# Kernel tuning notes

Hardware: AMD Instinct MI355X
Metric: run time of the kernel (lower is better)

The kernel has to match this reference:

```python
import jax, jax.numpy as jnp
import numpy as np

VAR0, VAR1 = 0.1, 0.2
THRESHOLD = 0.35
NEGPOS_RATIO = 7
LOW_GT_THRESH = 0.2  # match() filters GT whose best prior IoU < 0.2


def setup_inputs() -> dict:
    key = jax.random.key(0)
    ks = jax.random.split(key, 8)
    B, P, G = 16, 43008, 128
    loc_data = jax.random.normal(ks[0], (B, P, 4), jnp.float32)
    conf_data = jax.random.normal(ks[1], (B, P, 2), jnp.float32)
    landm_data = jax.random.normal(ks[2], (B, P, 10), jnp.float32)
    # priors in cxcywh form, positive sizes
    pc = jax.random.uniform(ks[3], (P, 2), jnp.float32)
    pwh = jax.random.uniform(ks[4], (P, 2), jnp.float32, minval=0.02, maxval=0.32)
    priors = jnp.concatenate([pc, pwh], axis=1)
    # targets: valid xyxy boxes + 10 landmark coords + label (face=1)
    ctr = jax.random.uniform(ks[5], (B, G, 2), jnp.float32, minval=0.2, maxval=0.8)
    wh = jax.random.uniform(ks[6], (B, G, 2), jnp.float32, minval=0.05, maxval=0.3)
    boxes = jnp.concatenate([ctr - wh / 2, ctr + wh / 2], axis=-1)
    landms = jax.random.uniform(ks[7], (B, G, 10), jnp.float32)
    labels = jnp.ones((B, G, 1), jnp.float32)
    targets = jnp.concatenate([boxes, landms, labels], axis=-1)
    return {"loc_data": loc_data, "conf_data": conf_data, "landm_data": landm_data,
            "priors": priors, "targets": targets}


def point_form(priors):
    return jnp.concatenate([priors[:, :2] - priors[:, 2:] / 2,
                            priors[:, :2] + priors[:, 2:] / 2], axis=1)


def jaccard(a, b):  # a: [G,4] xyxy, b: [P,4] xyxy -> [G,P]
    lt = jnp.maximum(a[:, None, :2], b[None, :, :2])
    rb = jnp.minimum(a[:, None, 2:], b[None, :, 2:])
    wh = jnp.clip(rb - lt, 0.0)
    inter = wh[..., 0] * wh[..., 1]
    area_a = (a[:, 2] - a[:, 0]) * (a[:, 3] - a[:, 1])
    area_b = (b[:, 2] - b[:, 0]) * (b[:, 3] - b[:, 1])
    return inter / (area_a[:, None] + area_b[None, :] - inter)


def encode(matched, priors):  # matched xyxy [P,4], priors cxcywh [P,4]
    g_cxcy = (matched[:, :2] + matched[:, 2:]) / 2 - priors[:, :2]
    g_cxcy = g_cxcy / (VAR0 * priors[:, 2:])
    g_wh = jnp.log((matched[:, 2:] - matched[:, :2]) / priors[:, 2:]) / VAR1
    return jnp.concatenate([g_cxcy, g_wh], axis=1)


def encode_landm(matched, priors):  # matched [P,10], priors [P,4]
    m = matched.reshape(-1, 5, 2)
    g = (m - priors[:, None, :2]) / (VAR0 * priors[:, None, 2:])
    return g.reshape(-1, 10)


def match_one(truths, labels, landms, priors):
    G = truths.shape[0]
    overlaps = jaccard(truths, point_form(priors))  # [G, P]
    best_prior_overlap = overlaps.max(axis=1)       # [G]
    best_prior_idx = overlaps.argmax(axis=1)        # [G]
    valid = best_prior_overlap >= LOW_GT_THRESH
    any_valid = jnp.any(valid)
    best_truth_overlap = overlaps.max(axis=0)       # [P]
    best_truth_idx = overlaps.argmax(axis=0)        # [P]
    # index_fill_(0, best_prior_idx_filter, 2): ensure each valid GT keeps its best prior
    fill_val = jnp.where(valid, 2.0, best_truth_overlap[best_prior_idx])
    best_truth_overlap = best_truth_overlap.at[best_prior_idx].set(fill_val)
    # best_truth_idx[best_prior_idx[j]] = j for all j
    best_truth_idx = best_truth_idx.at[best_prior_idx].set(jnp.arange(G))
    matches = truths[best_truth_idx]                       # [P,4]
    conf = labels[best_truth_idx].astype(jnp.int32)        # [P]
    conf = jnp.where(best_truth_overlap < THRESHOLD, 0, conf)
    conf = jnp.where(any_valid, conf, 0)  # no valid GT -> all background
    loc = encode(matches, priors)
    landm = encode_landm(landms[best_truth_idx], priors)
    return loc, conf, landm


def smooth_l1(x):
    ax = jnp.abs(x)
    return jnp.where(ax < 1.0, 0.5 * ax * ax, ax - 0.5)


def reference(loc_data, conf_data, landm_data, priors, targets):
    truths = targets[..., :4]
    landms = targets[..., 4:14]
    labels = targets[..., 14]
    loc_t, conf_t, landm_t = jax.vmap(
        lambda t, l, lm: match_one(t, l, lm, priors))(truths, labels, landms)

    # landmark loss over positives
    pos1 = conf_t > 0
    N1 = jnp.maximum(pos1.sum().astype(jnp.float32), 1.0)
    loss_landm = jnp.sum(smooth_l1(landm_data - landm_t) * pos1[..., None])

    # localization loss over positives
    pos = conf_t != 0
    num_pos = pos.sum(axis=1, keepdims=True)  # [B,1]
    loss_l = jnp.sum(smooth_l1(loc_data - loc_t) * pos[..., None])

    # hard negative mining on per-prior CE loss
    lse = jax.scipy.special.logsumexp(conf_data, axis=-1)  # [B,P]
    gathered = jnp.take_along_axis(conf_data, conf_t[..., None], axis=-1)[..., 0]
    ce_all = lse - gathered                                # [B,P] per-prior CE
    mine = jnp.where(pos, 0.0, ce_all)
    loss_idx = jnp.argsort(-mine, axis=1)
    idx_rank = jnp.argsort(loss_idx, axis=1)
    num_neg = jnp.clip(NEGPOS_RATIO * num_pos, None, pos.shape[1] - 1)
    neg = idx_rank < num_neg
    sel = pos | neg
    loss_c = jnp.sum(jnp.where(sel, ce_all, 0.0))

    N = jnp.maximum(num_pos.sum().astype(jnp.float32), 1.0)
    return loss_l / N, loss_c / N, loss_landm / N1
```

## Files before the change

### kernel.cpp

```cpp
#include <hip/hip_runtime.h>
#include <stdint.h>


#define GC 8
#define PPI 4
#define NCELL 1024

__device__ __forceinline__ float sl1(float x) {
  float a = fabsf(x);
  return a < 1.f ? 0.5f * a * a : a - 0.5f;
}

__device__ __forceinline__ double dwave(double v) {
#pragma unroll
  for (int o = 32; o; o >>= 1) v += __shfl_down(v, o);
  return v;
}

__device__ __forceinline__ int cellOf(float4 pr) {
  int cx = (int)(pr.x * 16.f); cx = cx < 0 ? 0 : (cx > 15 ? 15 : cx);
  int cy = (int)(pr.y * 16.f); cy = cy < 0 ? 0 : (cy > 15 ? 15 : cy);
  return ((cy * 16 + cx) << 2) | ((pr.z > 0.17f) ? 2 : 0) |
         ((pr.w > 0.17f) ? 1 : 0);
}

__device__ __forceinline__ unsigned bsufscan(unsigned x, unsigned* S,
                                             unsigned* wt, int tid) {
  int lane = tid & 63, wid = tid >> 6;
  unsigned v = x;
#pragma unroll
  for (int o = 1; o < 64; o <<= 1) {
    unsigned u = __shfl_down(v, o);
    if (lane + o < 64) v += u;
  }
  if (lane == 0) wt[wid] = v;
  __syncthreads();
  if (wid == 0) {
    unsigned tv = (lane < 16) ? wt[lane] : 0;
#pragma unroll
    for (int o = 1; o < 16; o <<= 1) {
      unsigned u = __shfl_down(tv, o);
      if (lane + o < 64) tv += u;
    }
    if (lane < 16) wt[lane] = tv;
  }
  __syncthreads();
  unsigned Sv = v + ((wid < 15) ? wt[wid + 1] : 0u);
  S[tid] = Sv;
  __syncthreads();
  return Sv;
}

__global__ __launch_bounds__(256) void k_hist(const float* __restrict__ priors,
                                              unsigned* __restrict__ cellh,
                                              int P) {
  int p = blockIdx.x * 256 + threadIdx.x;
  if (p < P) {
    float4 pr = ((const float4*)priors)[p];
    atomicAdd(&cellh[cellOf(pr)], 1u);
  }
}

__global__ __launch_bounds__(1024) void k_scan(const unsigned* __restrict__ cellh,
                                               unsigned* __restrict__ cellcur) {
  int tid = threadIdx.x;
  __shared__ unsigned s[NCELL];
  unsigned v = cellh[tid];
  s[tid] = v;
  __syncthreads();
  for (int off = 1; off < NCELL; off <<= 1) {
    unsigned a = (tid >= off) ? s[tid - off] : 0u;
    __syncthreads();
    s[tid] += a;
    __syncthreads();
  }
  cellcur[tid] = s[tid] - v;
}

__global__ __launch_bounds__(256) void k_scatter(
    const float* __restrict__ priors, unsigned* __restrict__ cellcur,
    float4* __restrict__ spr, unsigned* __restrict__ sid,
    unsigned* __restrict__ inv, int P) {
  int p = blockIdx.x * 256 + threadIdx.x;
  if (p < P) {
    float4 pr = ((const float4*)priors)[p];
    unsigned pos = atomicAdd(&cellcur[cellOf(pr)], 1u);
    spr[pos] = pr;
    sid[pos] = (unsigned)p;
    inv[p] = pos;
  }
}

__global__ __launch_bounds__(64) void k_wbox(const float4* __restrict__ spr,
                                             float4* __restrict__ wboxG, int P) {
  int p = blockIdx.x * 64 + threadIdx.x;
  float x1 = 1e30f, y1 = 1e30f, x2 = -1e30f, y2 = -1e30f;
  if (p < P) {
    float4 pr = spr[p];
    x1 = pr.x - pr.z * 0.5f; y1 = pr.y - pr.w * 0.5f;
    x2 = pr.x + pr.z * 0.5f; y2 = pr.y + pr.w * 0.5f;
  }
#pragma unroll
  for (int o = 32; o; o >>= 1) {
    x1 = fminf(x1, __shfl_down(x1, o));
    y1 = fminf(y1, __shfl_down(y1, o));
    x2 = fmaxf(x2, __shfl_down(x2, o));
    y2 = fmaxf(y2, __shfl_down(y2, o));
  }
  if (threadIdx.x == 0)
    wboxG[blockIdx.x] = make_float4(x1, y1, x2, y2);
}

__global__ __launch_bounds__(256) void k_gmask(
    const float4* __restrict__ wboxG, const float* __restrict__ targets,
    uint4* __restrict__ gmask, int G, int NRW, int NW) {
  int w = blockIdx.x * 4 + (threadIdx.x >> 6);
  int lane = threadIdx.x & 63;
  if (w >= NW) return;
  int b = w / NRW, run = w % NRW;
  float4 wb = wboxG[run];
  const float* t0 = targets + ((size_t)b * G + lane) * 15;
  const float* t1 = targets + ((size_t)b * G + lane + 64) * 15;
  bool o0, o1;
  {
    float gx1 = t0[0], gy1 = t0[1], gx2 = t0[2], gy2 = t0[3];
    o0 = (gx1 < wb.z) && (wb.x < gx2) && (gy1 < wb.w) && (wb.y < gy2);
  }
  {
    float gx1 = t1[0], gy1 = t1[1], gx2 = t1[2], gy2 = t1[3];
    o1 = (gx1 < wb.z) && (wb.x < gx2) && (gy1 < wb.w) && (wb.y < gy2);
  }
  unsigned long long b0 = __ballot(o0);
  unsigned long long b1 = __ballot(o1);
  if (lane == 0)
    gmask[(size_t)b * NRW + run] =
        make_uint4((unsigned)b0, (unsigned)(b0 >> 32), (unsigned)b1,
                   (unsigned)(b1 >> 32));
}

__global__ __launch_bounds__(256) void k_pconf(
    const float* __restrict__ conf, const unsigned* __restrict__ inv,
    float2* __restrict__ conf_s, int P) {
  int p = blockIdx.x * 256 + threadIdx.x;
  int b = blockIdx.y;
  if (p < P)
    conf_s[(size_t)b * P + inv[p]] = ((const float2*)conf)[(size_t)b * P + p];
}

__global__ __launch_bounds__(256) void k_mm(
    const float4* __restrict__ spr, const unsigned* __restrict__ sid,
    const uint4* __restrict__ gmask, const float2* __restrict__ conf_s,
    const float* __restrict__ targets, const float* __restrict__ loc,
    const float* __restrict__ lm, uint2* __restrict__ ovti,
    unsigned long long* __restrict__ bp, float* __restrict__ mine,
    unsigned* __restrict__ ghist, double* __restrict__ pll,
    double* __restrict__ pllm, double* __restrict__ plc,
    double* __restrict__ msum, int* __restrict__ pnp, int P, int G, int NIOU,
    int PTI, int NGC, int PC, int NRW) {
  int tid = threadIdx.x;
  __shared__ char smem[16384];
  __shared__ float4 sgt[128];
  __shared__ float sga[128];

  if ((int)blockIdx.x < NIOU) {
    float* st = (float*)smem;
    double* rs = (double*)(smem + 7680);
    int* ri = (int*)(smem + 7808);
    unsigned* hist = (unsigned*)(smem + 8192);
    unsigned* smaskw = (unsigned*)(smem + 12288);
    int b = blockIdx.x / PTI, tile = blockIdx.x % PTI;
    int base = tile * (256 * PPI);
    for (int i = tid; i < G * 15; i += 256)
      st[i] = targets[(size_t)b * G * 15 + i];
    for (int g = tid; g < G; g += 256) {
      const float* t = targets + ((size_t)b * G + g) * 15;
      float x1 = t[0], y1 = t[1], x2 = t[2], y2 = t[3];
      sgt[g] = make_float4(x1, y1, x2, y2);
      sga[g] = (x2 - x1) * (y2 - y1);
    }
    for (int i = tid; i < 1024; i += 256) hist[i] = 0;
    if (tid < 64)
      smaskw[tid] =
          ((const unsigned*)(gmask + (size_t)b * NRW + tile * 16))[tid];
    __syncthreads();

    float px1[PPI], py1[PPI], px2[PPI], py2[PPI], pa[PPI];
    float bi[PPI], sb[PPI];
    int bidx[PPI];
#pragma unroll
    for (int k = 0; k < PPI; ++k) {
      int p = base + tid + k * 256;
      int pl = p < P ? p : P - 1;
      float4 pr = spr[pl];
      px1[k] = pr.x - pr.z * 0.5f; py1[k] = pr.y - pr.w * 0.5f;
      px2[k] = pr.x + pr.z * 0.5f; py2[k] = pr.y + pr.w * 0.5f;
      pa[k] = pr.z * pr.w;
      bi[k] = 0.f; sb[k] = 1.f; bidx[k] = 0;
    }

#define IOU_UPD(GG)                                                        \
  {                                                                        \
    float iw = fminf(T.z, px2[k]) - fmaxf(T.x, px1[k]);                    \
    float ih = fminf(T.w, py2[k]) - fmaxf(T.y, py1[k]);                    \
    float inter = fmaxf(iw, 0.f) * ih;                                     \
    float S = A + pa[k];                                                   \
    if (inter * sb[k] > bi[k] * S) { bi[k] = inter; sb[k] = S; bidx[k] = (GG); } \
  }
#pragma unroll
    for (int k = 0; k < PPI; ++k) {
      int runl = k * 4 + (tid >> 6);
      unsigned mw0 = smaskw[runl * 4 + 0], mw1 = smaskw[runl * 4 + 1];
      unsigned mw2 = smaskw[runl * 4 + 2], mw3 = smaskw[runl * 4 + 3];
      unsigned long long m0 =
          ((unsigned long long)(unsigned)__builtin_amdgcn_readfirstlane(
               (int)mw1)
           << 32) |
          (unsigned)__builtin_amdgcn_readfirstlane((int)mw0);
      unsigned long long m1 =
          ((unsigned long long)(unsigned)__builtin_amdgcn_readfirstlane(
               (int)mw3)
           << 32) |
          (unsigned)__builtin_amdgcn_readfirstlane((int)mw2);
      while (m0) {
        int g = __builtin_ctzll(m0);
        m0 &= m0 - 1;
        float4 T = sgt[g];
        float A = sga[g];
        IOU_UPD(g)
      }
      while (m1) {
        int g = 64 + __builtin_ctzll(m1);
        m1 &= m1 - 1;
        float4 T = sgt[g];
        float A = sga[g];
        IOU_UPD(g)
      }
    }
#undef IOU_UPD

    double ll = 0, llm = 0, lc = 0, ms = 0;
    int np = 0;
#pragma unroll
    for (int k = 0; k < PPI; ++k) {
      int p = base + tid + k * 256;
      if (p < P) {
        size_t idxs = (size_t)b * P + p;
        float ov = bi[k] / (sb[k] - bi[k]);
        int ti = bidx[k];
        ovti[idxs] = make_uint2(__float_as_uint(ov), (unsigned)ti);
        bool pos = ov >= 0.35f;
        float2 c = conf_s[idxs];
        float mx = fmaxf(c.x, c.y);
        float dd = fabsf(c.x - c.y);
        float lse = mx + logf(1.f + expf(-dd));
        float ce = lse - (pos ? c.y : c.x);
        float mv = pos ? 0.f : ce;
        mine[idxs] = mv;
        atomicAdd(&hist[__float_as_uint(mv) >> 21], 1u);
        ms += (double)mv;
        if (pos) {
          np++;
          lc += (double)ce;
          float4 pr = spr[p];
          unsigned op = sid[p];
          size_t idxo = (size_t)b * P + op;
          const float* t = st + ti * 15;
          float rz = 1.f / pr.z, rw = 1.f / pr.w;
          float rdx = 10.f * rz, rdy = 10.f * rw;
          float gx = ((t[0] + t[2]) * 0.5f - pr.x) * rdx;
          float gy = ((t[1] + t[3]) * 0.5f - pr.y) * rdy;
          float gw = logf((t[2] - t[0]) * rz) * 5.0f;
          float gh = logf((t[3] - t[1]) * rw) * 5.0f;
          float4 ld = ((const float4*)loc)[idxo];
          ll += (double)(sl1(ld.x - gx) + sl1(ld.y - gy) + sl1(ld.z - gw) +
                         sl1(ld.w - gh));
          const float2* lmd = (const float2*)lm + idxo * 5;
          float s = 0.f;
#pragma unroll
          for (int j = 0; j < 5; ++j) {
            float2 lv = lmd[j];
            float ex = (t[4 + 2 * j] - pr.x) * rdx;
            float ey = (t[5 + 2 * j] - pr.y) * rdy;
            s += sl1(lv.x - ex) + sl1(lv.y - ey);
          }
          llm += (double)s;
        }
      }
    }

    ll = dwave(ll); llm = dwave(llm); lc = dwave(lc); ms = dwave(ms);
#pragma unroll
    for (int o = 32; o; o >>= 1) np += __shfl_down(np, o);
    int lane = tid & 63, wid = tid >> 6;
    if (lane == 0) {
      rs[wid] = ll; rs[4 + wid] = llm; rs[8 + wid] = lc; rs[12 + wid] = ms;
      ri[wid] = np;
    }
    __syncthreads();
    if (tid == 0) {
      pll[blockIdx.x] = rs[0] + rs[1] + rs[2] + rs[3];
      pllm[blockIdx.x] = rs[4] + rs[5] + rs[6] + rs[7];
      plc[blockIdx.x] = rs[8] + rs[9] + rs[10] + rs[11];
      msum[blockIdx.x] = rs[12] + rs[13] + rs[14] + rs[15];
      pnp[blockIdx.x] = ri[0] + ri[1] + ri[2] + ri[3];
    }
    for (int i = tid; i < 1024; i += 256) {
      unsigned c = hist[i];
      if (c) atomicAdd(&ghist[b * 1024 + i], c);
    }
  } else {
    unsigned long long* sred = (unsigned long long*)smem;
    unsigned char* bm = (unsigned char*)sga;
    int bc = blockIdx.x - NIOU;
    int pc = bc % PC;
    int gcb = (bc / PC) % NGC;
    int b = bc / (PC * NGC);
    int g0 = gcb * GC;

    int chunk = (P + PC - 1) / PC;
    int ps = pc * chunk;
    int pe = ps + chunk; if (pe > P) pe = P;
    int count = pe - ps;
    int nrun = (count + 63) >> 6;

    if (tid < GC) {
      int g = g0 + tid;
      float4 v = make_float4(0.f, 0.f, 0.f, 0.f);
      if (g < G) {
        const float* t = targets + ((size_t)b * G + g) * 15;
        v = make_float4(t[0], t[1], t[2], t[3]);
      }
      sgt[tid] = v;
    }
    if (tid < nrun) {
      uint4 m = gmask[(size_t)b * NRW + (ps >> 6) + tid];
      unsigned word = (g0 & 64) ? ((g0 & 32) ? m.w : m.z)
                                : ((g0 & 32) ? m.y : m.x);
      bm[tid] = (unsigned char)((word >> (g0 & 31)) & 0xffu);
    }
    __syncthreads();

    float gx1[GC], gy1[GC], gx2[GC], gy2[GC], ga[GC];
#pragma unroll
    for (int j = 0; j < GC; ++j) {
      float4 T = sgt[j];
      gx1[j] = T.x; gy1[j] = T.y; gx2[j] = T.z; gy2[j] = T.w;
      ga[j] = (T.z - T.x) * (T.w - T.y);
    }

    float bi[GC], sb[GC];
    unsigned bpp[GC];
#pragma unroll
    for (int j = 0; j < GC; ++j) { bi[j] = 0.f; sb[j] = 1.f; bpp[j] = 0xFFFFFFFFu; }

#define BP_BODY(X1, Y1, X2, Y2, AR, PP)                                     \
  {                                                                         \
    float iw = fminf(gx2[j], X2) - fmaxf(gx1[j], X1);                       \
    float ih = fminf(gy2[j], Y2) - fmaxf(gy1[j], Y1);                       \
    float inter = fmaxf(iw, 0.f) * ih;                                      \
    float S = ga[j] + AR;                                                   \
    if (inter * sb[j] > bi[j] * S) { bi[j] = inter; sb[j] = S; bpp[j] = (PP); } \
  }
    for (int i = tid; i < count; i += 1024) {
      int ib = __builtin_amdgcn_readfirstlane(i);
      int rl = ib >> 6;
      int i1 = i + 256, i2 = i + 512, i3 = i + 768;
      int p0 = ps + i;
      int p1 = (i1 < count) ? ps + i1 : p0;
      int p2 = (i2 < count) ? ps + i2 : p0;
      int p3 = (i3 < count) ? ps + i3 : p0;
      unsigned by0 = bm[rl];
      unsigned by1 = bm[(ib + 256 < count) ? rl + 4 : rl];
      unsigned by2 = bm[(ib + 512 < count) ? rl + 8 : rl];
      unsigned by3 = bm[(ib + 768 < count) ? rl + 12 : rl];
      by0 = (unsigned)__builtin_amdgcn_readfirstlane((int)by0);
      by1 = (unsigned)__builtin_amdgcn_readfirstlane((int)by1);
      by2 = (unsigned)__builtin_amdgcn_readfirstlane((int)by2);
      by3 = (unsigned)__builtin_amdgcn_readfirstlane((int)by3);
      float4 q0 = spr[p0];
      float4 q1 = spr[p1];
      float4 q2 = spr[p2];
      float4 q3 = spr[p3];
      unsigned s0 = sid[p0], s1 = sid[p1], s2 = sid[p2], s3 = sid[p3];
      float ax1 = q0.x - q0.z * 0.5f, ay1 = q0.y - q0.w * 0.5f;
      float ax2 = q0.x + q0.z * 0.5f, ay2 = q0.y + q0.w * 0.5f;
      float aa = q0.z * q0.w;
      float bx1 = q1.x - q1.z * 0.5f, by1f = q1.y - q1.w * 0.5f;
      float bx2 = q1.x + q1.z * 0.5f, by2f = q1.y + q1.w * 0.5f;
      float ba = q1.z * q1.w;
      float cx1 = q2.x - q2.z * 0.5f, cy1 = q2.y - q2.w * 0.5f;
      float cx2 = q2.x + q2.z * 0.5f, cy2 = q2.y + q2.w * 0.5f;
      float ca = q2.z * q2.w;
      float dx1 = q3.x - q3.z * 0.5f, dy1 = q3.y - q3.w * 0.5f;
      float dx2 = q3.x + q3.z * 0.5f, dy2 = q3.y + q3.w * 0.5f;
      float da = q3.z * q3.w;
#pragma unroll
      for (int j = 0; j < GC; ++j) {
        if (by0 & (1u << j)) BP_BODY(ax1, ay1, ax2, ay2, aa, s0)
        if (by1 & (1u << j)) BP_BODY(bx1, by1f, bx2, by2f, ba, s1)
        if (by2 & (1u << j)) BP_BODY(cx1, cy1, cx2, cy2, ca, s2)
        if (by3 & (1u << j)) BP_BODY(dx1, dy1, dx2, dy2, da, s3)
      }
    }
#undef BP_BODY

#pragma unroll
    for (int j = 0; j < GC; ++j) {
      float iou = bi[j] / (sb[j] - bi[j]);
      unsigned long long pk =
          ((unsigned long long)__float_as_uint(iou) << 32) | (unsigned)(~bpp[j]);
      sred[j * 256 + tid] = pk;
    }
    __syncthreads();
    {
      int j = tid >> 5, s = tid & 31;
      unsigned long long m = sred[j * 256 + s];
#pragma unroll
      for (int t = 1; t < 8; ++t) {
        unsigned long long v = sred[j * 256 + s + t * 32];
        if (v > m) m = v;
      }
      __syncthreads();
      sred[j * 256 + s] = m;
    }
    __syncthreads();
    if (tid < GC) {
      unsigned long long m = sred[tid * 256];
      for (int s = 1; s < 32; ++s) {
        unsigned long long v = sred[tid * 256 + s];
        if (v > m) m = v;
      }
      int g = g0 + tid;
      if (g < G) atomicMax(&bp[(size_t)b * G + g], m);
    }
  }
}

__global__ __launch_bounds__(1024) void k_tail2(
    const unsigned long long* __restrict__ bp, const unsigned* __restrict__ inv,
    uint2* __restrict__ ovti, const float* __restrict__ conf,
    const float* __restrict__ loc, const float* __restrict__ lm,
    const float* __restrict__ priors, const float* __restrict__ targets,
    float* __restrict__ mine, unsigned* __restrict__ ghist,
    const int* __restrict__ pnp, const double* __restrict__ msum,
    const double* __restrict__ pll, const double* __restrict__ pllm,
    const double* __restrict__ plc, double* __restrict__ gacc,
    int* __restrict__ gnp, unsigned* __restrict__ done,
    float* __restrict__ out, int P, int G, int PTI, int B) {
  int b = blockIdx.x, tid = threadIdx.x;
  int lane = tid & 63, wid = tid >> 6;
  __shared__ unsigned spp[128];
  __shared__ double rs[16 * 5];
  __shared__ int ris[16];
  __shared__ unsigned S[1024];
  __shared__ unsigned hs[2048];
  __shared__ unsigned wt[16];
  __shared__ double sdel[4];
  __shared__ int sdnp, sav, smode;
  __shared__ long long sk;
  __shared__ double sA, sC, sD;
  __shared__ int snpos;
  __shared__ int st_, sk1_;
  __shared__ unsigned lcnt;
  __shared__ int spf21, sk2;
  __shared__ unsigned stb;
  __shared__ double stie;

  double dll = 0, dllm = 0, dlc = 0, dms = 0;
  int dnp = 0;
  unsigned pp = 0;
  bool valid = false;
  if (tid < G) {
    unsigned long long m = bp[(size_t)b * G + tid];
    pp = (m == 0ull) ? 0u : ~(unsigned)m;
    float val = __uint_as_float((unsigned)(m >> 32));
    spp[tid] = pp;
    valid = val >= 0.2f;
  }
  int av = __syncthreads_or((tid < G && valid) ? 1 : 0);
  bool win = false;
  if (tid < G) {
    win = true;
    for (int g2 = tid + 1; g2 < G; ++g2)
      if (spp[g2] == pp) { win = false; break; }
  }
  if (win) {
    size_t idx = (size_t)b * P + pp;
    unsigned sp = inv[pp];
    size_t idxs = (size_t)b * P + sp;
    uint2 ot = ovti[idxs];
    float ov_o = __uint_as_float(ot.x);
    int ti_o = (int)ot.y;
    float ov_n = valid ? 2.0f : ov_o;
    int ti_n = tid;
    bool pos_o = ov_o >= 0.35f, pos_n = ov_n >= 0.35f;

    float2 c = ((const float2*)conf)[idx];
    float mx = fmaxf(c.x, c.y);
    float dd = fabsf(c.x - c.y);
    float lse = mx + logf(1.f + expf(-dd));
    float ce_o = lse - (pos_o ? c.y : c.x);
    float ce_n = lse - (pos_n ? c.y : c.x);
    float mv_o = mine[idxs];
    float mv_n = pos_n ? 0.f : ce_n;
    if (mv_n != mv_o) {
      mine[idxs] = mv_n;
      atomicSub(&ghist[b * 1024 + (__float_as_uint(mv_o) >> 21)], 1u);
      atomicAdd(&ghist[b * 1024 + (__float_as_uint(mv_n) >> 21)], 1u);
    }
    dms = (double)mv_n - (double)mv_o;
    dnp = (pos_n ? 1 : 0) - (pos_o ? 1 : 0);
    dlc = (pos_n ? (double)ce_n : 0.0) - (pos_o ? (double)ce_o : 0.0);

    if (pos_o || pos_n) {
      float4 pr = ((const float4*)priors)[pp];
      float rz = 1.f / pr.z, rw = 1.f / pr.w;
      float rdx = 10.f * rz, rdy = 10.f * rw;
      float4 ld = ((const float4*)loc)[idx];
      const float2* lmd = (const float2*)lm + idx * 5;
      float2 lv[5];
#pragma unroll
      for (int j = 0; j < 5; ++j) lv[j] = lmd[j];
      for (int pass = 0; pass < 2; ++pass) {
        bool act = pass ? pos_n : pos_o;
        int ti = pass ? ti_n : ti_o;
        if (!act) continue;
        const float* t = targets + ((size_t)b * G + ti) * 15;
        float gx = ((t[0] + t[2]) * 0.5f - pr.x) * rdx;
        float gy = ((t[1] + t[3]) * 0.5f - pr.y) * rdy;
        float gw = logf((t[2] - t[0]) * rz) * 5.0f;
        float gh = logf((t[3] - t[1]) * rw) * 5.0f;
        double l = (double)(sl1(ld.x - gx) + sl1(ld.y - gy) +
                            sl1(ld.z - gw) + sl1(ld.w - gh));
        float s = 0.f;
#pragma unroll
        for (int j = 0; j < 5; ++j) {
          float ex = (t[4 + 2 * j] - pr.x) * rdx;
          float ey = (t[5 + 2 * j] - pr.y) * rdy;
          s += sl1(lv[j].x - ex) + sl1(lv[j].y - ey);
        }
        if (pass) { dll += l; dllm += (double)s; }
        else { dll -= l; dllm -= (double)s; }
      }
    }
  }
  dll = dwave(dll); dllm = dwave(dllm); dlc = dwave(dlc); dms = dwave(dms);
#pragma unroll
  for (int o = 32; o; o >>= 1) dnp += __shfl_down(dnp, o);
  if (lane == 0) {
    rs[wid] = dll; rs[16 + wid] = dllm; rs[32 + wid] = dlc; rs[48 + wid] = dms;
    ris[wid] = dnp;
  }
  __syncthreads();
  if (tid == 0) {
    double a = 0, c2 = 0, d2 = 0, m2 = 0;
    int n2 = 0;
    for (int i = 0; i < 16; ++i) {
      a += rs[i]; c2 += rs[16 + i]; d2 += rs[32 + i]; m2 += rs[48 + i];
      n2 += ris[i];
    }
    sdel[0] = a; sdel[1] = c2; sdel[2] = d2; sdel[3] = m2;
    sdnp = n2; sav = av;
  }
  __syncthreads();

  double a = 0, cc = 0, d = 0, ms = 0;
  int n = 0;
  for (int i = tid; i < PTI; i += 1024) {
    int ix = b * PTI + i;
    a += pll[ix]; cc += pllm[ix]; d += plc[ix]; ms += msum[ix]; n += pnp[ix];
  }
  a = dwave(a); cc = dwave(cc); d = dwave(d); ms = dwave(ms);
#pragma unroll
  for (int o = 32; o; o >>= 1) n += __shfl_down(n, o);
  if (lane == 0) {
    rs[wid] = a; rs[16 + wid] = cc; rs[32 + wid] = d; rs[48 + wid] = ms;
    ris[wid] = n;
  }
  __syncthreads();
  double Fv = 0.0;
  if (tid == 0) {
    double A = 0, C = 0, D = 0, MS = 0;
    int npos = 0;
    for (int i = 0; i < 16; ++i) {
      A += rs[i]; C += rs[16 + i]; D += rs[32 + i]; MS += rs[48 + i];
      npos += ris[i];
    }
    A += sdel[0]; C += sdel[1]; D += sdel[2]; MS += sdel[3];
    npos += sdnp;
    if (!sav) { A = 0; C = 0; D = 0; npos = 0; }
    sA = A; sC = C; sD = D; snpos = npos;
    long long k = 7LL * (long long)npos;
    long long cap = P - 1;
    int md = 1;
    if (k <= 0) { Fv = 0.0; md = 0; }
    else if (k >= cap) { Fv = MS; md = 0; }
    smode = md; sk = k;
  }
  __syncthreads();

  if (smode) {
    long long k = sk;
    {
      unsigned x = ghist[b * 1024 + tid];
      unsigned Sv = bsufscan(x, S, wt, tid);
      int cnt_ = __syncthreads_count((long long)Sv >= k);
      int seg = cnt_ - 1;
      if (tid == seg) {
        long long cum = (seg + 1 < 1024) ? (long long)S[seg + 1] : 0;
        st_ = seg;
        sk1_ = (int)(k - cum);
      }
      if (tid == 0) lcnt = 0;
    }
    __syncthreads();
    int t = st_;
    long long k1 = (long long)sk1_;

    const float* mrow = mine + (size_t)b * P;
    float* crow = (float*)(ovti + (size_t)b * P);
    double acc = 0;
    for (int base0 = 0; base0 < P; base0 += 1024) {
      int p = base0 + tid;
      bool keep = false;
      unsigned bb = 0;
      if (p < P) {
        bb = __float_as_uint(mrow[p]);
        int bin = (int)(bb >> 21);
        if (bin > t) acc += (double)__uint_as_float(bb);
        else keep = (bin == t);
      }
      unsigned long long mk = __ballot(keep);
      int nset = __popcll(mk);
      if (nset) {
        unsigned wbase = 0;
        if (lane == 0) wbase = atomicAdd(&lcnt, (unsigned)nset);
        wbase = __shfl(wbase, 0);
        if (keep) {
          int offi = __popcll(mk & ((1ull << lane) - 1ull));
          crow[wbase + offi] = __uint_as_float(bb);
        }
      }
    }
    acc = dwave(acc);
    if (lane == 0) rs[wid] = acc;
    __syncthreads();
    int nn = (int)lcnt;

    hs[tid] = 0; hs[tid + 1024] = 0;
    __syncthreads();
    for (int i = tid; i < nn; i += 1024) {
      unsigned bb = __float_as_uint(crow[i]);
      atomicAdd(&hs[(bb >> 10) & 2047], 1u);
    }
    __syncthreads();
    {
      unsigned h0 = hs[tid * 2], h1v = hs[tid * 2 + 1];
      unsigned Sv = bsufscan(h0 + h1v, S, wt, tid);
      int cnt_ = __syncthreads_count((long long)Sv >= k1);
      int seg = cnt_ - 1;
      if (tid == seg) {
        long long cum = (seg + 1 < 1024) ? (long long)S[seg + 1] : 0;
        int bin = seg * 2;
        if (cum + h1v >= k1) bin = seg * 2 + 1;
        else cum += h1v;
        spf21 = (t << 11) | bin;
        sk2 = (int)(k1 - cum);
      }
    }
    __syncthreads();
    int pf21 = spf21;

    hs[tid] = 0;
    __syncthreads();
    for (int i = tid; i < nn; i += 1024) {
      unsigned bb = __float_as_uint(crow[i]);
      if ((int)(bb >> 10) == pf21) atomicAdd(&hs[bb & 1023], 1u);
    }
    __syncthreads();
    {
      unsigned Sv = bsufscan(hs[tid], S, wt, tid);
      long long kk = (long long)sk2;
      int cnt_ = __syncthreads_count((long long)Sv >= kk);
      int seg = cnt_ - 1;
      if (tid == seg) {
        long long cum = (seg + 1 < 1024) ? (long long)S[seg + 1] : 0;
        unsigned tb = ((unsigned)pf21 << 10) | (unsigned)seg;
        stb = tb;
        stie = (double)(kk - cum) * (double)__uint_as_float(tb);
      }
    }
    __syncthreads();

    unsigned tb = stb;
    double v = 0.0;
    for (int i = tid; i < nn; i += 1024) {
      unsigned bb = __float_as_uint(crow[i]);
      if (bb > tb) v += (double)__uint_as_float(bb);
    }
    v = dwave(v);
    if (lane == 0) rs[16 + wid] = v;
    __syncthreads();
    if (tid == 0) {
      double hi = 0, vt = 0;
      for (int i = 0; i < 16; ++i) { hi += rs[i]; vt += rs[16 + i]; }
      Fv = hi + vt + stie;
    }
  }

  if (tid == 0) {
    atomicAdd(&gacc[0], sA);
    atomicAdd(&gacc[1], sC);
    atomicAdd(&gacc[2], sD);
    atomicAdd(&gacc[3], Fv);
    atomicAdd(gnp, snpos);
    __threadfence();
    unsigned old = atomicAdd(done, 1u);
    if (old == (unsigned)B - 1) {
      __threadfence();
      double A = atomicAdd(&gacc[0], 0.0);
      double C = atomicAdd(&gacc[1], 0.0);
      double D = atomicAdd(&gacc[2], 0.0);
      double F = atomicAdd(&gacc[3], 0.0);
      int N = atomicAdd(gnp, 0);
      double Nd = N < 1 ? 1.0 : (double)N;
      out[0] = (float)(A / Nd);
      out[1] = (float)((D + F) / Nd);
      out[2] = (float)(C / Nd);
    }
  }
}

extern "C" void kernel_launch(void* const* d_in, const int* in_sizes, int n_in,
                              void* d_out, int out_size, void* d_ws,
                              size_t ws_size, hipStream_t stream) {
  const float* loc = (const float*)d_in[0];
  const float* conf = (const float*)d_in[1];
  const float* lm = (const float*)d_in[2];
  const float* priors = (const float*)d_in[3];
  const float* targets = (const float*)d_in[4];

  int P = in_sizes[3] / 4;
  int B = in_sizes[0] / (4 * P);
  int G = in_sizes[4] / (15 * B);
  int PTI = (P + 256 * PPI - 1) / (256 * PPI);
  int NIOU = B * PTI;
  int NGC = (G + GC - 1) / GC;
  int PC = 8;
  int NBP = B * NGC * PC;
  int NPB = (P + 255) / 256;
  int NRW = (P + 63) / 64;
  int NW = B * NRW;

  char* w = (char*)d_ws;
  size_t off = 0;
  unsigned long long* bp = (unsigned long long*)(w + off);
  off += (size_t)B * G * 8;
  unsigned* ghist = (unsigned*)(w + off);
  off += (size_t)B * 1024 * 4;
  unsigned* cellh = (unsigned*)(w + off);
  off += (size_t)NCELL * 4;
  double* gacc = (double*)(w + off);
  off += 4 * 8;
  int* gnp = (int*)(w + off);
  off += 4;
  unsigned* done = (unsigned*)(w + off);
  off += 4;
  size_t clear_bytes = off;
  off = (off + 255) & ~(size_t)255;
  float4* spr = (float4*)(w + off);
  off += (size_t)NRW * 64 * 16;
  unsigned* sid = (unsigned*)(w + off);
  off += (size_t)P * 4;
  unsigned* inv = (unsigned*)(w + off);
  off += (size_t)P * 4;
  float4* wboxG = (float4*)(w + off);
  off += (size_t)NRW * 16;
  uint4* gmask = (uint4*)(w + off);
  off += (size_t)NW * 16;
  unsigned* cellcur = (unsigned*)(w + off);
  off += (size_t)NCELL * 4;
  off = (off + 255) & ~(size_t)255;
  float2* conf_s = (float2*)(w + off);
  off += (size_t)B * P * 8;
  uint2* ovti = (uint2*)(w + off);
  off += (size_t)B * P * 8;
  float* mine = (float*)(w + off);
  off += (size_t)B * P * 4;
  double* pll = (double*)(w + off);
  off += (size_t)NIOU * 8;
  double* pllm = (double*)(w + off);
  off += (size_t)NIOU * 8;
  double* plc = (double*)(w + off);
  off += (size_t)NIOU * 8;
  double* msum = (double*)(w + off);
  off += (size_t)NIOU * 8;
  int* pnp = (int*)(w + off);
  off += (size_t)NIOU * 4;

  hipMemsetAsync(d_ws, 0, clear_bytes, stream);

  k_hist<<<NPB, 256, 0, stream>>>(priors, cellh, P);
  k_scan<<<1, 1024, 0, stream>>>(cellh, cellcur);
  k_scatter<<<NPB, 256, 0, stream>>>(priors, cellcur, spr, sid, inv, P);
  k_wbox<<<NRW, 64, 0, stream>>>(spr, wboxG, P);
  k_gmask<<<(NW + 3) / 4, 256, 0, stream>>>(wboxG, targets, gmask, G, NRW, NW);
  {
    dim3 gp((unsigned)((P + 255) / 256), (unsigned)B);
    k_pconf<<<gp, 256, 0, stream>>>(conf, inv, conf_s, P);
  }
  k_mm<<<NIOU + NBP, 256, 0, stream>>>(spr, sid, gmask, conf_s, targets, loc,
                                       lm, ovti, bp, mine, ghist, pll, pllm,
                                       plc, msum, pnp, P, G, NIOU, PTI, NGC,
                                       PC, NRW);
  k_tail2<<<B, 1024, 0, stream>>>(bp, inv, ovti, conf, loc, lm, priors,
                                  targets, mine, ghist, pnp, msum, pll, pllm,
                                  plc, gacc, gnp, done, (float*)d_out, P, G,
                                  PTI, B);
}
```

Before: 197.6 us.

## Fuse window-box and gmask kernels, drop conf permutation, halve priors per thread

```diff
diff --git a/kernel.cpp b/kernel.cpp
--- a/kernel.cpp
+++ b/kernel.cpp
@@ -3,7 +3,7 @@
 
 
 #define GC 8
-#define PPI 4
+#define PPI 2
 #define NCELL 1024
 
 __device__ __forceinline__ float sl1(float x) {
@@ -91,9 +91,14 @@
   }
 }
 
-__global__ __launch_bounds__(64) void k_wbox(const float4* __restrict__ spr,
-                                             float4* __restrict__ wboxG, int P) {
-  int p = blockIdx.x * 64 + threadIdx.x;
+__global__ __launch_bounds__(64) void k_wgm(
+    const float4* __restrict__ spr, const float* __restrict__ targets,
+    uint4* __restrict__ gmask, unsigned* __restrict__ zbase, int zwords,
+    int G, int NRW, int B, int P) {
+  int run = blockIdx.x, lane = threadIdx.x;
+  for (int i = run * 64 + lane; i < zwords; i += NRW * 64) zbase[i] = 0u;
+
+  int p = run * 64 + lane;
   float x1 = 1e30f, y1 = 1e30f, x2 = -1e30f, y2 = -1e30f;
   if (p < P) {
     float4 pr = spr[p];
@@ -107,49 +112,26 @@
     x2 = fmaxf(x2, __shfl_down(x2, o));
     y2 = fmaxf(y2, __shfl_down(y2, o));
   }
-  if (threadIdx.x == 0)
-    wboxG[blockIdx.x] = make_float4(x1, y1, x2, y2);
-}
-
-__global__ __launch_bounds__(256) void k_gmask(
-    const float4* __restrict__ wboxG, const float* __restrict__ targets,
-    uint4* __restrict__ gmask, int G, int NRW, int NW) {
-  int w = blockIdx.x * 4 + (threadIdx.x >> 6);
-  int lane = threadIdx.x & 63;
-  if (w >= NW) return;
-  int b = w / NRW, run = w % NRW;
-  float4 wb = wboxG[run];
-  const float* t0 = targets + ((size_t)b * G + lane) * 15;
-  const float* t1 = targets + ((size_t)b * G + lane + 64) * 15;
-  bool o0, o1;
-  {
-    float gx1 = t0[0], gy1 = t0[1], gx2 = t0[2], gy2 = t0[3];
-    o0 = (gx1 < wb.z) && (wb.x < gx2) && (gy1 < wb.w) && (wb.y < gy2);
-  }
-  {
-    float gx1 = t1[0], gy1 = t1[1], gx2 = t1[2], gy2 = t1[3];
-    o1 = (gx1 < wb.z) && (wb.x < gx2) && (gy1 < wb.w) && (wb.y < gy2);
-  }
-  unsigned long long b0 = __ballot(o0);
-  unsigned long long b1 = __ballot(o1);
-  if (lane == 0)
-    gmask[(size_t)b * NRW + run] =
-        make_uint4((unsigned)b0, (unsigned)(b0 >> 32), (unsigned)b1,
-                   (unsigned)(b1 >> 32));
-}
-
-__global__ __launch_bounds__(256) void k_pconf(
-    const float* __restrict__ conf, const unsigned* __restrict__ inv,
-    float2* __restrict__ conf_s, int P) {
-  int p = blockIdx.x * 256 + threadIdx.x;
-  int b = blockIdx.y;
-  if (p < P)
-    conf_s[(size_t)b * P + inv[p]] = ((const float2*)conf)[(size_t)b * P + p];
+  x1 = __shfl(x1, 0); y1 = __shfl(y1, 0);
+  x2 = __shfl(x2, 0); y2 = __shfl(y2, 0);
+
+  for (int b = 0; b < B; ++b) {
+    const float* t0 = targets + ((size_t)b * G + lane) * 15;
+    const float* t1 = targets + ((size_t)b * G + lane + 64) * 15;
+    bool o0 = (t0[0] < x2) && (x1 < t0[2]) && (t0[1] < y2) && (y1 < t0[3]);
+    bool o1 = (t1[0] < x2) && (x1 < t1[2]) && (t1[1] < y2) && (y1 < t1[3]);
+    unsigned long long b0 = __ballot(o0);
+    unsigned long long b1 = __ballot(o1);
+    if (lane == 0)
+      gmask[(size_t)b * NRW + run] =
+          make_uint4((unsigned)b0, (unsigned)(b0 >> 32), (unsigned)b1,
+                     (unsigned)(b1 >> 32));
+  }
 }
 
 __global__ __launch_bounds__(256) void k_mm(
     const float4* __restrict__ spr, const unsigned* __restrict__ sid,
-    const uint4* __restrict__ gmask, const float2* __restrict__ conf_s,
+    const uint4* __restrict__ gmask, const float* __restrict__ conf,
     const float* __restrict__ targets, const float* __restrict__ loc,
     const float* __restrict__ lm, uint2* __restrict__ ovti,
     unsigned long long* __restrict__ bp, float* __restrict__ mine,
@@ -179,9 +161,9 @@
       sga[g] = (x2 - x1) * (y2 - y1);
     }
     for (int i = tid; i < 1024; i += 256) hist[i] = 0;
-    if (tid < 64)
+    if (tid < 8 * 4)
       smaskw[tid] =
-          ((const unsigned*)(gmask + (size_t)b * NRW + tile * 16))[tid];
+          ((const unsigned*)(gmask + (size_t)b * NRW + tile * (4 * PPI)))[tid];
     __syncthreads();
 
     float px1[PPI], py1[PPI], px2[PPI], py2[PPI], pa[PPI];
@@ -249,7 +231,9 @@
         int ti = bidx[k];
         ovti[idxs] = make_uint2(__float_as_uint(ov), (unsigned)ti);
         bool pos = ov >= 0.35f;
-        float2 c = conf_s[idxs];
+        unsigned op = sid[p];
+        size_t idxo = (size_t)b * P + op;
+        float2 c = ((const float2*)conf)[idxo];
         float mx = fmaxf(c.x, c.y);
         float dd = fabsf(c.x - c.y);
         float lse = mx + logf(1.f + expf(-dd));
@@ -262,8 +246,6 @@
           np++;
           lc += (double)ce;
           float4 pr = spr[p];
-          unsigned op = sid[p];
-          size_t idxo = (size_t)b * P + op;
           const float* t = st + ti * 15;
           float rz = 1.f / pr.z, rw = 1.f / pr.w;
           float rdx = 10.f * rz, rdy = 10.f * rw;
@@ -620,25 +602,28 @@
     const float* mrow = mine + (size_t)b * P;
     float* crow = (float*)(ovti + (size_t)b * P);
     double acc = 0;
-    for (int base0 = 0; base0 < P; base0 += 1024) {
-      int p = base0 + tid;
-      bool keep = false;
-      unsigned bb = 0;
-      if (p < P) {
-        bb = __float_as_uint(mrow[p]);
-        int bin = (int)(bb >> 21);
-        if (bin > t) acc += (double)__uint_as_float(bb);
-        else keep = (bin == t);
-      }
-      unsigned long long mk = __ballot(keep);
-      int nset = __popcll(mk);
-      if (nset) {
-        unsigned wbase = 0;
-        if (lane == 0) wbase = atomicAdd(&lcnt, (unsigned)nset);
-        wbase = __shfl(wbase, 0);
-        if (keep) {
-          int offi = __popcll(mk & ((1ull << lane) - 1ull));
-          crow[wbase + offi] = __uint_as_float(bb);
+    for (int base0 = 0; base0 < P; base0 += 4096) {
+#pragma unroll
+      for (int j = 0; j < 4; ++j) {
+        int p = base0 + tid + j * 1024;
+        bool keep = false;
+        unsigned bb = 0;
+        if (p < P) {
+          bb = __float_as_uint(mrow[p]);
+          int bin = (int)(bb >> 21);
+          if (bin > t) acc += (double)__uint_as_float(bb);
+          else keep = (bin == t);
+        }
+        unsigned long long mk = __ballot(keep);
+        int nset = __popcll(mk);
+        if (nset) {
+          unsigned wbase = 0;
+          if (lane == 0) wbase = atomicAdd(&lcnt, (unsigned)nset);
+          wbase = __shfl(wbase, 0);
+          if (keep) {
+            int offi = __popcll(mk & ((1ull << lane) - 1ull));
+            crow[wbase + offi] = __uint_as_float(bb);
+          }
         }
       }
     }
@@ -758,8 +743,6 @@
   off += (size_t)B * G * 8;
   unsigned* ghist = (unsigned*)(w + off);
   off += (size_t)B * 1024 * 4;
-  unsigned* cellh = (unsigned*)(w + off);
-  off += (size_t)NCELL * 4;
   double* gacc = (double*)(w + off);
   off += 4 * 8;
   int* gnp = (int*)(w + off);
@@ -774,15 +757,13 @@
   off += (size_t)P * 4;
   unsigned* inv = (unsigned*)(w + off);
   off += (size_t)P * 4;
-  float4* wboxG = (float4*)(w + off);
-  off += (size_t)NRW * 16;
   uint4* gmask = (uint4*)(w + off);
   off += (size_t)NW * 16;
+  unsigned* cellh = (unsigned*)(w + off);
+  off += (size_t)NCELL * 4;
   unsigned* cellcur = (unsigned*)(w + off);
   off += (size_t)NCELL * 4;
   off = (off + 255) & ~(size_t)255;
-  float2* conf_s = (float2*)(w + off);
-  off += (size_t)B * P * 8;
   uint2* ovti = (uint2*)(w + off);
   off += (size_t)B * P * 8;
   float* mine = (float*)(w + off);
@@ -798,18 +779,14 @@
   int* pnp = (int*)(w + off);
   off += (size_t)NIOU * 4;
 
-  hipMemsetAsync(d_ws, 0, clear_bytes, stream);
+  hipMemsetAsync(cellh, 0, (size_t)NCELL * 4, stream);
 
   k_hist<<<NPB, 256, 0, stream>>>(priors, cellh, P);
   k_scan<<<1, 1024, 0, stream>>>(cellh, cellcur);
   k_scatter<<<NPB, 256, 0, stream>>>(priors, cellcur, spr, sid, inv, P);
-  k_wbox<<<NRW, 64, 0, stream>>>(spr, wboxG, P);
-  k_gmask<<<(NW + 3) / 4, 256, 0, stream>>>(wboxG, targets, gmask, G, NRW, NW);
-  {
-    dim3 gp((unsigned)((P + 255) / 256), (unsigned)B);
-    k_pconf<<<gp, 256, 0, stream>>>(conf, inv, conf_s, P);
-  }
-  k_mm<<<NIOU + NBP, 256, 0, stream>>>(spr, sid, gmask, conf_s, targets, loc,
+  k_wgm<<<NRW, 64, 0, stream>>>(spr, targets, gmask, (unsigned*)w,
+                                (int)(clear_bytes / 4), G, NRW, B, P);
+  k_mm<<<NIOU + NBP, 256, 0, stream>>>(spr, sid, gmask, conf, targets, loc,
                                        lm, ovti, bp, mine, ghist, pll, pllm,
                                        plc, msum, pnp, P, G, NIOU, PTI, NGC,
                                        PC, NRW);
```

Result: slower. 202.5 us (+2.5%).
